# Kernel optimization log

Hardware: AMD Instinct MI355X
Metric: run time of the kernel (lower is better)

## Reference

```python
import jax, jax.numpy as jnp
import numpy as np
from jax import lax

S, B, T, H, FH, FU = 8, 256, 90, 256, 14, 76
IN_H, IN_F, IN_U = 16, 16, 4


def _cell(x, h, c, Wih, Whh, b):
    # x:[S,B,in] h,c:[S,B,H] Wih:[S,4H,in] Whh:[S,4H,H] b:[S,4H]
    g = jnp.einsum('sbi,sgi->sbg', x, Wih) + jnp.einsum('sbh,sgh->sbg', h, Whh) + b[:, None, :]
    i, f, gg, o = jnp.split(g, 4, axis=-1)
    c = jax.nn.sigmoid(f) * c + jax.nn.sigmoid(i) * jnp.tanh(gg)
    h = jax.nn.sigmoid(o) * jnp.tanh(c)
    return h, c


def _encode(x_seq, params):
    # x_seq:[T,S,B,in]; stacked LSTM, zero initial state (torch nn.LSTM default)
    hs, cs = [], []
    inp = x_seq
    for (Wih, Whh, b) in params:
        h0 = jnp.zeros((x_seq.shape[1], x_seq.shape[2], Whh.shape[-1]), x_seq.dtype)

        def step(carry, x, Wih=Wih, Whh=Whh, b=b):
            h, c = _cell(x, carry[0], carry[1], Wih, Whh, b)
            return (h, c), h

        (h, c), inp = lax.scan(step, (h0, h0), inp)
        hs.append(h); cs.append(c)
    return jnp.stack(hs), jnp.stack(cs)  # [L,S,B,H]


def _decode(x_seq, params, h0, c0, level, win, wout, gW, gb, adj, flow_std):
    L = len(params)

    def step(carry, x):
        hs, cs, lev = carry
        inp = x
        nh, nc = [], []
        for l in range(L):
            h, c = _cell(inp, hs[l], cs[l], *params[l])
            inp = h; nh.append(h); nc.append(c)
        # headers_in: Linear(H+1 -> H, no bias) + ReLU (dropout is eval no-op)
        feat = jnp.concatenate([inp, lev], axis=-1)            # [S,B,H+1]
        hin = jax.nn.relu(jnp.einsum('sbf,shf->sbh', feat, win))
        # GraphConvolution: adj @ (X W) + b over the site axis
        graphed = jnp.einsum('st,tbk->sbk', adj, jnp.einsum('sbh,hk->sbk', hin, gW)) + gb
        # headers_out: ReLU + Linear(H -> 1, no bias)
        flow = jnp.einsum('sbh,soh->sbo', jax.nn.relu(graphed), wout)  # [S,B,1]
        lev = lev + flow * flow_std[:, None, None]
        return (jnp.stack(nh), jnp.stack(nc), lev), flow[..., 0]
    (hs, cs, lev), flows = lax.scan(step, (h0, c0, level), x_seq)
    return hs, cs, lev, flows  # flows: [T,S,B]


def setup_inputs() -> dict:
    key = jax.random.key(0)
    ks = iter(jax.random.split(key, 40))
    sc = 1.0 / np.sqrt(H)

    def u(shape):
        return jax.random.uniform(next(ks), shape, jnp.float32, -sc, sc)

    inp = {
        'x_d': jax.random.normal(next(ks), (S, B, T, IN_H), jnp.float32),
        'x_f': jax.random.normal(next(ks), (S, B, FH, IN_F), jnp.float32),
        'x_ff': jax.random.normal(next(ks), (S, B, FU, IN_U), jnp.float32),
        'level0': jax.random.uniform(next(ks), (S, B, 1), jnp.float32),
        'flow_std': jax.random.uniform(next(ks), (S,), jnp.float32, 0.5, 2.0),
    }
    # adjacency: chain edges + self loops (diag=True, digraph=False)
    adj = np.zeros((S, S), dtype=np.float32)
    for i in range(S - 1):
        adj[i, i + 1] = 1.0
    adj += np.eye(S, dtype=np.float32)
    inp['adj'] = jnp.asarray(adj)
    for pfx, in0 in [('enc', IN_H), ('df', IN_F), ('du', IN_U)]:
        inp[pfx + '_Wih0'] = u((S, 4 * H, in0))
        inp[pfx + '_Whh0'] = u((S, 4 * H, H))
        inp[pfx + '_b0'] = u((S, 4 * H))
        inp[pfx + '_Wih1'] = u((S, 4 * H, H))
        inp[pfx + '_Whh1'] = u((S, 4 * H, H))
        inp[pfx + '_b1'] = u((S, 4 * H))
    inp['win'] = u((S, H, H + 1))
    inp['wout'] = u((S, 1, H))
    inp['gW'] = u((H, H))
    inp['gb'] = u((H,))
    return inp


def reference(x_d, x_f, x_ff, level0, flow_std, adj,
              enc_Wih0, enc_Whh0, enc_b0, enc_Wih1, enc_Whh1, enc_b1,
              df_Wih0, df_Whh0, df_b0, df_Wih1, df_Whh1, df_b1,
              du_Wih0, du_Whh0, du_b0, du_Wih1, du_Whh1, du_b1,
              win, wout, gW, gb):
    enc_p = [(enc_Wih0, enc_Whh0, enc_b0), (enc_Wih1, enc_Whh1, enc_b1)]
    df_p = [(df_Wih0, df_Whh0, df_b0), (df_Wih1, df_Whh1, df_b1)]
    du_p = [(du_Wih0, du_Whh0, du_b0), (du_Wih1, du_Whh1, du_b1)]
    # encode historic sequence per site
    h, c = _encode(jnp.transpose(x_d, (2, 0, 1, 3)), enc_p)
    # forecast-horizon decode with graph mixing each step
    h, c, lev, f1 = _decode(jnp.transpose(x_f, (2, 0, 1, 3)), df_p, h, c,
                            level0, win, wout, gW, gb, adj, flow_std)
    # future-horizon decode continues from the same state
    h, c, lev, f2 = _decode(jnp.transpose(x_ff, (2, 0, 1, 3)), du_p, h, c,
                            lev, win, wout, gW, gb, adj, flow_std)
    flows = jnp.concatenate([f1, f2], axis=0)      # [FH+FU, S, B]
    return jnp.transpose(flows, (2, 0, 1))         # [B, target_horizon, S]
```

## Files before the change

kernel.cpp:

```cpp
#include <hip/hip_runtime.h>

typedef unsigned short u16;
typedef __bf16 bf16_t;
typedef bf16_t bf16x8 __attribute__((ext_vector_type(8)));
typedef float f32x4 __attribute__((ext_vector_type(4)));
typedef unsigned int u32x4 __attribute__((ext_vector_type(4)));

#define DEV static __device__ __forceinline__

DEV u16 f2bf(float f){ unsigned u = __float_as_uint(f); return (u16)((u + 0x7fffu + ((u>>16)&1u))>>16); }
DEV float bf2f(u16 b){ return __uint_as_float(((unsigned)b)<<16); }
DEV float sigf(float x){ return 1.0f/(1.0f+__expf(-x)); }
DEV float tanhf_(float x){ float e = __expf(2.0f*x); return 1.0f - 2.0f/(e+1.0f); }

union FragU { bf16x8 v; u16 u[8]; u32x4 q; };

DEV void ldg16_nw(u32x4 r[16], const void* b0, const void* b1){
  asm volatile(
    "global_load_dwordx4 %0,  %16, off sc0 sc1\n\t"
    "global_load_dwordx4 %1,  %16, off offset:64 sc0 sc1\n\t"
    "global_load_dwordx4 %2,  %16, off offset:128 sc0 sc1\n\t"
    "global_load_dwordx4 %3,  %16, off offset:192 sc0 sc1\n\t"
    "global_load_dwordx4 %4,  %16, off offset:256 sc0 sc1\n\t"
    "global_load_dwordx4 %5,  %16, off offset:320 sc0 sc1\n\t"
    "global_load_dwordx4 %6,  %16, off offset:384 sc0 sc1\n\t"
    "global_load_dwordx4 %7,  %16, off offset:448 sc0 sc1\n\t"
    "global_load_dwordx4 %8,  %17, off sc0 sc1\n\t"
    "global_load_dwordx4 %9,  %17, off offset:64 sc0 sc1\n\t"
    "global_load_dwordx4 %10, %17, off offset:128 sc0 sc1\n\t"
    "global_load_dwordx4 %11, %17, off offset:192 sc0 sc1\n\t"
    "global_load_dwordx4 %12, %17, off offset:256 sc0 sc1\n\t"
    "global_load_dwordx4 %13, %17, off offset:320 sc0 sc1\n\t"
    "global_load_dwordx4 %14, %17, off offset:384 sc0 sc1\n\t"
    "global_load_dwordx4 %15, %17, off offset:448 sc0 sc1"
    : "=&v"(r[0]), "=&v"(r[1]), "=&v"(r[2]), "=&v"(r[3]),
      "=&v"(r[4]), "=&v"(r[5]), "=&v"(r[6]), "=&v"(r[7]),
      "=&v"(r[8]), "=&v"(r[9]), "=&v"(r[10]), "=&v"(r[11]),
      "=&v"(r[12]), "=&v"(r[13]), "=&v"(r[14]), "=&v"(r[15])
    : "v"(b0), "v"(b1)
    : "memory");
}
DEV void wait_vm16(){ asm volatile("s_waitcnt vmcnt(16)" ::: "memory"); __builtin_amdgcn_sched_barrier(0); }
DEV void wait_vm0(){ asm volatile("s_waitcnt vmcnt(0)" ::: "memory"); __builtin_amdgcn_sched_barrier(0); }

DEV void ldg8f_sc(u32x4 r[8], float& lv, const void* b0, const float* lp){
  asm volatile(
    "global_load_dwordx4 %0, %9, off sc0 sc1\n\t"
    "global_load_dwordx4 %1, %9, off offset:64 sc0 sc1\n\t"
    "global_load_dwordx4 %2, %9, off offset:128 sc0 sc1\n\t"
    "global_load_dwordx4 %3, %9, off offset:192 sc0 sc1\n\t"
    "global_load_dwordx4 %4, %9, off offset:256 sc0 sc1\n\t"
    "global_load_dwordx4 %5, %9, off offset:320 sc0 sc1\n\t"
    "global_load_dwordx4 %6, %9, off offset:384 sc0 sc1\n\t"
    "global_load_dwordx4 %7, %9, off offset:448 sc0 sc1\n\t"
    "global_load_dword %8, %10, off sc0 sc1\n\t"
    "s_waitcnt vmcnt(0)"
    : "=&v"(r[0]), "=&v"(r[1]), "=&v"(r[2]), "=&v"(r[3]),
      "=&v"(r[4]), "=&v"(r[5]), "=&v"(r[6]), "=&v"(r[7]), "=&v"(lv)
    : "v"(b0), "v"(lp)
    : "memory");
}
DEV float ldf_sc(const float* p){
  float r;
  asm volatile("global_load_dword %0, %1, off sc0 sc1\n\ts_waitcnt vmcnt(0)"
               : "=&v"(r) : "v"(p) : "memory");
  return r;
}
DEV void stg16_sc(void* p, u32x4 v){
  asm volatile("global_store_dwordx4 %0, %1, off sc0 sc1" :: "v"(p), "v"(v) : "memory");
}
DEV void stf_sc(float* p, float v){
  asm volatile("global_store_dword %0, %1, off sc0 sc1" :: "v"(p), "v"(v) : "memory");
}

struct PArgs {
  const u16 *whh0[3], *wih0p[3], *whh1[3], *wih1[3];
  const float *b0[3], *b1[3];
  const float *x[3];
  const u16 *winH; const float *winLev;
  const u16 *gT;
  const float *gb, *wout, *adj, *fstd;
  u16 *h0a, *h0b, *h1a, *h1b;
  u16 *hgA, *hgB;
  float *levA, *levB;
  float *out;
  unsigned *bar;
  int T[3]; int IN[3];
};

#define RLX __ATOMIC_RELAXED
#define AGT __HIP_MEMORY_SCOPE_AGENT

DEV void gsync_site(unsigned* cnt, unsigned gen){
  asm volatile("s_waitcnt vmcnt(0)" ::: "memory");
  __syncthreads();
  if (threadIdx.x == 0){
    __hip_atomic_fetch_add(cnt, 1u, RLX, AGT);
    unsigned tgt = gen * 32u;
    while (__hip_atomic_load(cnt, RLX, AGT) < tgt) __builtin_amdgcn_s_sleep(1);
  }
  __syncthreads();
}

DEV void gsync_glob(unsigned* bar, int s, bool leader, unsigned gen, unsigned ggen){
  asm volatile("s_waitcnt vmcnt(0)" ::: "memory");
  __syncthreads();
  if (threadIdx.x == 0){
    unsigned* cnt  = bar + s*64;
    unsigned* rel  = bar + 512 + s*64;
    unsigned* root = bar + 1024;
    __hip_atomic_fetch_add(cnt, 1u, RLX, AGT);
    if (leader){
      while (__hip_atomic_load(cnt, RLX, AGT) < gen*32u) __builtin_amdgcn_s_sleep(1);
      __hip_atomic_fetch_add(root, 1u, RLX, AGT);
      while (__hip_atomic_load(root, RLX, AGT) < ggen*8u) __builtin_amdgcn_s_sleep(1);
      __hip_atomic_store(rel, ggen, RLX, AGT);
    } else {
      while (__hip_atomic_load(rel, RLX, AGT) < ggen) __builtin_amdgcn_s_sleep(1);
    }
  }
  __syncthreads();
}

DEV void pinW256(const u16* Wsite, int gt, u16* lds, int tid){
#pragma unroll
  for (int it = 0; it < 8; ++it){
    int flat = it*512 + tid;
    int n = flat >> 5, ks = flat & 31;
    int j = (n >> 5)*256 + gt*32 + (n & 31);
    bf16x8 v = *reinterpret_cast<const bf16x8*>(Wsite + (size_t)j*256 + ks*8);
    int sl = ks ^ (n & 7);
    *reinterpret_cast<bf16x8*>(lds + n*256 + sl*8) = v;
  }
}
DEV void pinWp(const u16* wpSite, int gt, u16* lds, int tid){
  int n = tid >> 2, ks = tid & 3;
  int j = (n >> 5)*256 + gt*32 + (n & 31);
  bf16x8 v = *reinterpret_cast<const bf16x8*>(wpSite + (size_t)j*32 + ks*8);
  int sl = ks ^ (n & 3);
  *reinterpret_cast<bf16x8*>(lds + n*32 + sl*8) = v;
}
DEV void pinWin(const u16* winH, int s, int gt, u16* lds, int tid){
#pragma unroll
  for (int it = 0; it < 2; ++it){
    int flat = it*512 + tid;
    int nn = flat >> 5, ks = flat & 31;
    bf16x8 v = *reinterpret_cast<const bf16x8*>(winH + ((size_t)s*256 + gt*32 + nn)*256 + ks*8);
    int sl = ks ^ (nn & 7);
    *reinterpret_cast<bf16x8*>(lds + nn*256 + sl*8) = v;
  }
}

DEV void seg_mfma(const u16* ldsW, const u32x4 a[16], f32x4 acc[2][4],
                  int l15, int l4, int nh){
#pragma unroll
  for (int ck = 0; ck < 8; ++ck){
#pragma unroll
    for (int mf = 0; mf < 2; ++mf){
      FragU af; af.q = a[mf*8 + ck];
#pragma unroll
      for (int q = 0; q < 4; ++q){
        int n = q*32 + nh*16 + l15;
        int sl = (ck*4 + l4) ^ (n & 7);
        acc[mf][q] = __builtin_amdgcn_mfma_f32_16x16x32_bf16(
            af.v, *reinterpret_cast<const bf16x8*>(ldsW + n*256 + sl*8), acc[mf][q], 0,0,0);
      }
    }
  }
}

DEV void cell_epi2(const float bb[4], float* cR, u16* hOutSite,
                   int rowBase, int hcb, int lane, u16* wscr, const f32x4 acc[2][4]){
  int l15 = lane & 15, l4 = lane >> 4;
#pragma unroll
  for (int mf = 0; mf < 2; ++mf)
#pragma unroll
    for (int r = 0; r < 4; ++r){
      float gi = acc[mf][0][r] + bb[0];
      float gf = acc[mf][1][r] + bb[1];
      float gg = acc[mf][2][r] + bb[2];
      float go = acc[mf][3][r] + bb[3];
      float cn = sigf(gf)*cR[mf*4+r] + sigf(gi)*tanhf_(gg);
      cR[mf*4+r] = cn;
      wscr[(mf*16 + l4*4 + r)*16 + l15] = f2bf(sigf(go)*tanhf_(cn));
    }
  asm volatile("s_waitcnt lgkmcnt(0)" ::: "memory");
  u32x4 v = *reinterpret_cast<const u32x4*>(wscr + lane*8);
  stg16_sc(hOutSite + (size_t)(rowBase + (lane>>1))*256 + hcb + (lane&1)*8, v);
}

__global__ __launch_bounds__(512, 2) void k_persist(PArgs A){
  extern __shared__ char smem[];
  u16* lds0 = (u16*)smem;
  u16* lds1 = (u16*)(smem + 65536);
  u16* ldsWin = (u16*)(smem + 65536 + 8192);
  u16* scratch = (u16*)(smem + 131072);
  float (*red)[16] = (float(*)[16])(smem + 139264);

  const int bid = blockIdx.x, tid = threadIdx.x;
  const int w = tid >> 6, lane = tid & 63, l15 = lane & 15, l4 = lane >> 4;
  const int s = bid & 7, fam = (bid >> 3) & 1, sub = bid >> 4;
  const int bt = sub & 1, gt = sub >> 1;
  const int mt = w & 3, nh = w >> 2;
  const int rowBase = bt*128 + mt*32;
  const int hcb = gt*32 + nh*16;
  const size_t sOff = (size_t)s*65536;
  const bool leader = (bid < 8);
  unsigned* siteCnt = A.bar + s*64;
  u16* wscr = scratch + w*512;

  float cR[8];
#pragma unroll
  for (int i = 0; i < 8; ++i) cR[i] = 0.f;

  unsigned gen = 0, ggen = 0;
  const int gb0[3] = {0, 90, 104};

  for (int ph = 0; ph < 3; ++ph){
    const int T = A.T[ph];
    const int IN = A.IN[ph];
    const bool dec = (ph > 0);
    const int SS = T + (dec ? 3 : 1);
    const int tdb = (ph == 2) ? 14 : 0;

    float bb[4];
    if (fam == 0){
      pinW256(A.whh0[ph] + (size_t)s*262144, gt, lds0, tid);
      pinWp  (A.wih0p[ph] + (size_t)s*32768, gt, lds1, tid);
      pinWin (A.winH, s, gt, ldsWin, tid);
      const float* bS = A.b0[ph] + s*1024;
#pragma unroll
      for (int g = 0; g < 4; ++g) bb[g] = bS[g*256 + hcb + l15];
    } else {
      pinW256(A.whh1[ph] + (size_t)s*262144, gt, lds0, tid);
      pinW256(A.wih1[ph] + (size_t)s*262144, gt, lds1, tid);
      const float* bS = A.b1[ph] + s*1024;
#pragma unroll
      for (int g = 0; g < 4; ++g) bb[g] = bS[g*256 + hcb + l15];
    }
    __syncthreads();

    for (int ss = 0; ss < SS; ++ss){
      if (fam == 0){
        if (ss < T){
          int t = ss, g0 = gb0[ph] + t;
          const u16* h0in = ((g0 & 1) ? A.h0b : A.h0a) + sOff;
          u16* h0out = ((g0 & 1) ? A.h0a : A.h0b) + sOff;
          f32x4 acc[2][4];
#pragma unroll
          for (int mf = 0; mf < 2; ++mf)
#pragma unroll
            for (int q = 0; q < 4; ++q) acc[mf][q] = (f32x4){0.f,0.f,0.f,0.f};
          u32x4 a[16];
          ldg16_nw(a, h0in + (size_t)(rowBase + l15)*256 + l4*8,
                      h0in + (size_t)(rowBase + 16 + l15)*256 + l4*8);
          FragU xa[2];
#pragma unroll
          for (int mf = 0; mf < 2; ++mf){
#pragma unroll
            for (int e = 0; e < 8; ++e) xa[mf].u[e] = 0;
            const float* xrow = A.x[ph] + ((size_t)(s*256 + rowBase + mf*16 + l15)*T + t)*IN;
            if (IN == 16){
              if (l4 < 2){
                float4 u0 = reinterpret_cast<const float4*>(xrow)[l4*2];
                float4 u1 = reinterpret_cast<const float4*>(xrow)[l4*2+1];
                xa[mf].u[0]=f2bf(u0.x); xa[mf].u[1]=f2bf(u0.y); xa[mf].u[2]=f2bf(u0.z); xa[mf].u[3]=f2bf(u0.w);
                xa[mf].u[4]=f2bf(u1.x); xa[mf].u[5]=f2bf(u1.y); xa[mf].u[6]=f2bf(u1.z); xa[mf].u[7]=f2bf(u1.w);
              }
            } else {
              if (l4 == 0){
                float4 u0 = *reinterpret_cast<const float4*>(xrow);
                xa[mf].u[0]=f2bf(u0.x); xa[mf].u[1]=f2bf(u0.y); xa[mf].u[2]=f2bf(u0.z); xa[mf].u[3]=f2bf(u0.w);
              }
            }
          }
          wait_vm0();
          seg_mfma(lds0, a, acc, l15, l4, nh);
#pragma unroll
          for (int mf = 0; mf < 2; ++mf)
#pragma unroll
            for (int q = 0; q < 4; ++q){
              int n = q*32 + nh*16 + l15;
              int sl = l4 ^ (n & 3);
              acc[mf][q] = __builtin_amdgcn_mfma_f32_16x16x32_bf16(
                  xa[mf].v, *reinterpret_cast<const bf16x8*>(lds1 + n*32 + sl*8), acc[mf][q], 0,0,0);
            }
          cell_epi2(bb, cR, h0out, rowBase, hcb, lane, wscr, acc);
        }
        if (dec){
          int th = ss - 2;
          if (th >= 0 && th < T){
            int g = gb0[ph] + th, tdec = tdb + th;
            const u16* h1cur = ((g & 1) ? A.h1a : A.h1b) + sOff;
            u16* hg = ((tdec & 1) ? A.hgB : A.hgA) + sOff;
            f32x4 a2[2];
            a2[0] = (f32x4){0.f,0.f,0.f,0.f}; a2[1] = a2[0];
            u32x4 a[16];
            ldg16_nw(a, h1cur + (size_t)(rowBase + l15)*256 + l4*8,
                        h1cur + (size_t)(rowBase + 16 + l15)*256 + l4*8);
            wait_vm0();
#pragma unroll
            for (int ck = 0; ck < 8; ++ck)
#pragma unroll
              for (int mf = 0; mf < 2; ++mf){
                FragU af; af.q = a[mf*8 + ck];
                int n = nh*16 + l15;
                int sl = (ck*4 + l4) ^ (n & 7);
                a2[mf] = __builtin_amdgcn_mfma_f32_16x16x32_bf16(
                    af.v, *reinterpret_cast<const bf16x8*>(ldsWin + n*256 + sl*8), a2[mf], 0,0,0);
              }
#pragma unroll
            for (int mf = 0; mf < 2; ++mf)
#pragma unroll
              for (int r = 0; r < 4; ++r)
                wscr[(mf*16 + l4*4 + r)*16 + l15] = f2bf(a2[mf][r]);
            asm volatile("s_waitcnt lgkmcnt(0)" ::: "memory");
            u32x4 v = *reinterpret_cast<const u32x4*>(wscr + lane*8);
            stg16_sc(hg + (size_t)(rowBase + (lane>>1))*256 + hcb + (lane&1)*8, v);
          }
        }
      } else {
        int t = ss - 1;
        if (t >= 0 && t < T){
          int g = gb0[ph] + t;
          const u16* h1in = ((g & 1) ? A.h1b : A.h1a) + sOff;
          u16* h1out = ((g & 1) ? A.h1a : A.h1b) + sOff;
          const u16* h0cur = ((g & 1) ? A.h0a : A.h0b) + sOff;
          f32x4 acc[2][4];
#pragma unroll
          for (int mf = 0; mf < 2; ++mf)
#pragma unroll
            for (int q = 0; q < 4; ++q) acc[mf][q] = (f32x4){0.f,0.f,0.f,0.f};
          u32x4 a0[16], a1[16];
          ldg16_nw(a0, h1in + (size_t)(rowBase + l15)*256 + l4*8,
                       h1in + (size_t)(rowBase + 16 + l15)*256 + l4*8);
          ldg16_nw(a1, h0cur + (size_t)(rowBase + l15)*256 + l4*8,
                       h0cur + (size_t)(rowBase + 16 + l15)*256 + l4*8);
          wait_vm16();
          seg_mfma(lds0, a0, acc, l15, l4, nh);
          wait_vm0();
          seg_mfma(lds1, a1, acc, l15, l4, nh);
          cell_epi2(bb, cR, h1out, rowBase, hcb, lane, wscr, acc);
        }
        if (dec){
          int tgl = ss - 3;
          if (tgl >= 0 && tgl < T){
            int tg = tdb + tgl;
            const u16* hgb16 = (tg & 1) ? A.hgB : A.hgA;
            const float* levc = (tg & 1) ? A.levB : A.levA;
            float* levn = (tg & 1) ? A.levA : A.levB;
            int brow0 = sub*16;
            f32x4 acc[2];
            acc[0] = (f32x4){0.f,0.f,0.f,0.f}; acc[1] = acc[0];
            for (int ts = 0; ts < 8; ++ts){
              float av = A.adj[s*8 + ts];
              if (av == 0.f) continue;
              float lv;
              u32x4 hv[8];
              ldg8f_sc(hv, lv, hgb16 + (size_t)ts*65536 + (size_t)(brow0 + l15)*256 + l4*8,
                       levc + ts*256 + brow0 + l15);
              const float* wlB = A.winLev + ts*256 + l4*8;
#pragma unroll
              for (int ck = 0; ck < 8; ++ck){
                FragU hr; hr.q = hv[ck];
                float4 w0 = *reinterpret_cast<const float4*>(wlB + ck*32);
                float4 w1 = *reinterpret_cast<const float4*>(wlB + ck*32 + 4);
                float wls[8] = {w0.x,w0.y,w0.z,w0.w,w1.x,w1.y,w1.z,w1.w};
                FragU af;
#pragma unroll
                for (int e = 0; e < 8; ++e)
                  af.u[e] = f2bf(fmaxf(bf2f(hr.u[e]) + lv*wls[e], 0.f) * av);
#pragma unroll
                for (int q = 0; q < 2; ++q){
                  int n = (w*2+q)*16 + l15;
                  bf16x8 bfr = *reinterpret_cast<const bf16x8*>(A.gT + (size_t)n*256 + ck*32 + l4*8);
                  acc[q] = __builtin_amdgcn_mfma_f32_16x16x32_bf16(af.v, bfr, acc[q], 0,0,0);
                }
              }
            }
            float part[4] = {0.f,0.f,0.f,0.f};
            const float* woS = A.wout + s*256;
#pragma unroll
            for (int q = 0; q < 2; ++q){
              int m = (w*2+q)*16 + l15;
              float gbv = A.gb[m], wo = woS[m];
#pragma unroll
              for (int r = 0; r < 4; ++r) part[r] += fmaxf(acc[q][r] + gbv, 0.f) * wo;
            }
#pragma unroll
            for (int d = 1; d < 16; d <<= 1)
#pragma unroll
              for (int r = 0; r < 4; ++r) part[r] += __shfl_xor(part[r], d, 64);
            if (l15 == 0)
#pragma unroll
              for (int r = 0; r < 4; ++r) red[w][l4*4+r] = part[r];
            __syncthreads();
            if (tid < 16){
              float flow = 0.f;
#pragma unroll
              for (int ww = 0; ww < 8; ++ww) flow += red[ww][tid];
              int b = brow0 + tid;
              A.out[(size_t)b*720 + tg*8 + s] = flow;
              float lvo = ldf_sc(levc + s*256 + b);
              stf_sc(levn + s*256 + b, lvo + flow * A.fstd[s]);
            }
          }
        }
      }
      ++gen;
      if (dec){ ++ggen; gsync_glob(A.bar, s, leader, gen, ggen); }
      else     gsync_site(siteCnt, gen);
    }
  }
}

struct Cvt9Args { const float* s[9]; u16* d[9]; };
__global__ void k_cvt9(Cvt9Args A){
  size_t i = (size_t)blockIdx.x*256 + threadIdx.x;
  int t = (int)(i >> 21); size_t r = i & 2097151u;
  A.d[t][r] = f2bf(A.s[t][r]);
}
struct Pad3Args { const float* s[3]; u16* d[3]; int kx[3]; };
__global__ void k_pad3(Pad3Args A){
  size_t i = (size_t)blockIdx.x*256 + threadIdx.x;
  int t = (int)(i >> 18); int r = (int)(i & 262143u);
  int row = r >> 5, col = r & 31;
  int kx = A.kx[t];
  A.d[t][r] = (col < kx) ? f2bf(A.s[t][(size_t)row*kx + col]) : (u16)0;
}
__global__ void k_win(const float* win, u16* winH, float* winLev){
  size_t i = (size_t)blockIdx.x*256 + threadIdx.x;
  if (i >= (size_t)8*256*257) return;
  int k = (int)(i % 257); size_t sm = i / 257;
  float v = win[i];
  if (k < 256) winH[sm*256 + k] = f2bf(v);
  else winLev[sm] = v;
}
__global__ void k_gt(const float* gW, u16* gT){
  int i = blockIdx.x*256 + threadIdx.x;
  int h = i >> 8, k = i & 255;
  gT[(size_t)k*256 + h] = f2bf(gW[i]);
}

extern "C" void kernel_launch(void* const* d_in, const int* in_sizes, int n_in,
                              void* d_out, int out_size, void* d_ws, size_t ws_size,
                              hipStream_t stream){
  const float* x_d    = (const float*)d_in[0];
  const float* x_f    = (const float*)d_in[1];
  const float* x_ff   = (const float*)d_in[2];
  const float* level0 = (const float*)d_in[3];
  const float* fstd   = (const float*)d_in[4];
  const float* adj    = (const float*)d_in[5];
  const float* W[18];
  for (int i = 0; i < 18; i++) W[i] = (const float*)d_in[6+i];
  const float* win  = (const float*)d_in[24];
  const float* wout = (const float*)d_in[25];
  const float* gW   = (const float*)d_in[26];
  const float* gb   = (const float*)d_in[27];

  char* base = (char*)d_ws;
  size_t off = 0;
  auto alloc = [&](size_t bytes)->void*{
    void* r = base + off;
    off += (bytes + 255) & ~(size_t)255;
    return r;
  };
  u16* wb[9]; for (int i = 0; i < 9; i++) wb[i] = (u16*)alloc((size_t)2097152*2);
  u16* wp[3]; for (int i = 0; i < 3; i++) wp[i] = (u16*)alloc((size_t)262144*2);
  u16* winH = (u16*)alloc((size_t)524288*2);
  u16* gT   = (u16*)alloc((size_t)65536*2);
  float* winLev = (float*)alloc((size_t)2048*4);
  u16* h0a = (u16*)alloc((size_t)524288*2);
  u16* h0b = (u16*)alloc((size_t)524288*2);
  u16* h1a = (u16*)alloc((size_t)524288*2);
  u16* h1b = (u16*)alloc((size_t)524288*2);
  u16* hgA = (u16*)alloc((size_t)524288*2);
  u16* hgB = (u16*)alloc((size_t)524288*2);
  float* levA = (float*)alloc((size_t)2048*4);
  float* levB = (float*)alloc((size_t)2048*4);
  unsigned* bar = (unsigned*)alloc(8192);

  Cvt9Args c9;
  const float* c9s[9] = { W[1], W[4], W[3],  W[7], W[10], W[9],  W[13], W[16], W[15] };
  for (int i = 0; i < 9; i++){ c9.s[i] = c9s[i]; c9.d[i] = wb[i]; }
  k_cvt9<<<73728,256,0,stream>>>(c9);

  Pad3Args p3;
  const float* p3s[3] = { W[0], W[6], W[12] };
  int kx3[3] = {16,16,4};
  for (int i = 0; i < 3; i++){ p3.s[i] = p3s[i]; p3.d[i] = wp[i]; p3.kx[i] = kx3[i]; }
  k_pad3<<<3072,256,0,stream>>>(p3);

  k_win<<<2057,256,0,stream>>>(win, winH, winLev);
  k_gt<<<256,256,0,stream>>>(gW, gT);

  (void)hipMemsetAsync(h0a, 0, (size_t)524288*2, stream);
  (void)hipMemsetAsync(h1a, 0, (size_t)524288*2, stream);
  (void)hipMemsetAsync(bar, 0, 8192, stream);
  (void)hipMemcpyAsync(levA, level0, (size_t)2048*4, hipMemcpyDeviceToDevice, stream);

  PArgs A;
  for (int ph = 0; ph < 3; ++ph){
    A.whh0[ph] = wb[ph*3+0];
    A.whh1[ph] = wb[ph*3+1];
    A.wih1[ph] = wb[ph*3+2];
    A.wih0p[ph] = wp[ph];
  }
  A.b0[0] = W[2];  A.b1[0] = W[5];
  A.b0[1] = W[8];  A.b1[1] = W[11];
  A.b0[2] = W[14]; A.b1[2] = W[17];
  A.x[0] = x_d; A.x[1] = x_f; A.x[2] = x_ff;
  A.winH = winH; A.winLev = winLev;
  A.gT = gT; A.gb = gb; A.wout = wout; A.adj = adj; A.fstd = fstd;
  A.h0a = h0a; A.h0b = h0b; A.h1a = h1a; A.h1b = h1b;
  A.hgA = hgA; A.hgB = hgB;
  A.levA = levA; A.levB = levB;
  A.out = (float*)d_out;
  A.bar = bar;
  A.T[0] = 90; A.T[1] = 14; A.T[2] = 76;
  A.IN[0] = 16; A.IN[1] = 16; A.IN[2] = 4;

  const int smemBytes = 139776;
  (void)hipFuncSetAttribute((const void*)k_persist, hipFuncAttributeMaxDynamicSharedMemorySize, smemBytes);
  k_persist<<<dim3(256), dim3(512), smemBytes, stream>>>(A);
}
```

Measured before the change: 3.328 ms.

## Replace global/site barriers with fine-grained dependency counters per site and batch half

Replaces the per-step site barrier and the two-level global barrier with per-(site, batch-half, family) arrival counters. At the start of each step, one wavefront polls only the counters its work depends on: its own site, plus the neighbouring site during decode, following the graph and layer data flow. This is meant to cut the cost of an all-to-all barrier on each of the 90+ recurrent steps and let independent groups run ahead. It depends on the dependency sets being complete, and a missing edge would cause a race.

```diff
diff --git a/kernel.cpp b/kernel.cpp
--- a/kernel.cpp
+++ b/kernel.cpp
@@ -7,6 +7,8 @@
 typedef unsigned int u32x4 __attribute__((ext_vector_type(4)));
 
 #define DEV static __device__ __forceinline__
+#define RLX __ATOMIC_RELAXED
+#define AGT __HIP_MEMORY_SCOPE_AGENT
 
 DEV u16 f2bf(float f){ unsigned u = __float_as_uint(f); return (u16)((u + 0x7fffu + ((u>>16)&1u))>>16); }
 DEV float bf2f(u16 b){ return __uint_as_float(((unsigned)b)<<16); }
@@ -57,8 +59,7 @@
     "s_waitcnt vmcnt(0)"
     : "=&v"(r[0]), "=&v"(r[1]), "=&v"(r[2]), "=&v"(r[3]),
       "=&v"(r[4]), "=&v"(r[5]), "=&v"(r[6]), "=&v"(r[7]), "=&v"(lv)
-    : "v"(b0), "v"(lp)
-    : "memory");
+    : "v"(b0), "v"(lp) : "memory");
 }
 DEV float ldf_sc(const float* p){
   float r;
@@ -71,6 +72,12 @@
 }
 DEV void stf_sc(float* p, float v){
   asm volatile("global_store_dword %0, %1, off sc0 sc1" :: "v"(p), "v"(v) : "memory");
+}
+DEV unsigned ld_spin_ic(const unsigned* p){
+  unsigned r;
+  asm volatile("global_load_dword %0, %1, off sc0 sc1\n\ts_waitcnt vmcnt(0)"
+               : "=&v"(r) : "v"(p) : "memory");
+  return r;
 }
 
 struct PArgs {
@@ -88,40 +95,6 @@
   int T[3]; int IN[3];
 };
 
-#define RLX __ATOMIC_RELAXED
-#define AGT __HIP_MEMORY_SCOPE_AGENT
-
-DEV void gsync_site(unsigned* cnt, unsigned gen){
-  asm volatile("s_waitcnt vmcnt(0)" ::: "memory");
-  __syncthreads();
-  if (threadIdx.x == 0){
-    __hip_atomic_fetch_add(cnt, 1u, RLX, AGT);
-    unsigned tgt = gen * 32u;
-    while (__hip_atomic_load(cnt, RLX, AGT) < tgt) __builtin_amdgcn_s_sleep(1);
-  }
-  __syncthreads();
-}
-
-DEV void gsync_glob(unsigned* bar, int s, bool leader, unsigned gen, unsigned ggen){
-  asm volatile("s_waitcnt vmcnt(0)" ::: "memory");
-  __syncthreads();
-  if (threadIdx.x == 0){
-    unsigned* cnt  = bar + s*64;
-    unsigned* rel  = bar + 512 + s*64;
-    unsigned* root = bar + 1024;
-    __hip_atomic_fetch_add(cnt, 1u, RLX, AGT);
-    if (leader){
-      while (__hip_atomic_load(cnt, RLX, AGT) < gen*32u) __builtin_amdgcn_s_sleep(1);
-      __hip_atomic_fetch_add(root, 1u, RLX, AGT);
-      while (__hip_atomic_load(root, RLX, AGT) < ggen*8u) __builtin_amdgcn_s_sleep(1);
-      __hip_atomic_store(rel, ggen, RLX, AGT);
-    } else {
-      while (__hip_atomic_load(rel, RLX, AGT) < ggen) __builtin_amdgcn_s_sleep(1);
-    }
-  }
-  __syncthreads();
-}
-
 DEV void pinW256(const u16* Wsite, int gt, u16* lds, int tid){
 #pragma unroll
   for (int it = 0; it < 8; ++it){
@@ -196,6 +169,7 @@
   u16* ldsWin = (u16*)(smem + 65536 + 8192);
   u16* scratch = (u16*)(smem + 131072);
   float (*red)[16] = (float(*)[16])(smem + 139264);
+  __shared__ unsigned pollE[8], pollD[8];
 
   const int bid = blockIdx.x, tid = threadIdx.x;
   const int w = tid >> 6, lane = tid & 63, l15 = lane & 15, l4 = lane >> 4;
@@ -205,15 +179,40 @@
   const int rowBase = bt*128 + mt*32;
   const int hcb = gt*32 + nh*16;
   const size_t sOff = (size_t)s*65536;
-  const bool leader = (bid < 8);
-  unsigned* siteCnt = A.bar + s*64;
   u16* wscr = scratch + w*512;
 
+  auto offA = [](int ss, int bb){ return (unsigned)((ss*2 + bb)*64); };
+  auto offB = [](int ss, int bb){ return (unsigned)(1024 + (ss*2 + bb)*64); };
+  if (tid == 0){
+    pollE[0] = offA(s, bt); pollE[1] = offB(s, bt);
+#pragma unroll
+    for (int i = 2; i < 8; ++i) pollE[i] = pollE[0];
+    if (fam == 0){
+      pollD[0] = offA(s, bt);
+      pollD[1] = offB(s, 0); pollD[2] = offB(s, 1);
+      pollD[3] = (s > 0) ? offB(s-1, 0) : pollD[0];
+      pollD[4] = (s > 0) ? offB(s-1, 1) : pollD[0];
+      pollD[5] = pollD[0]; pollD[6] = pollD[0]; pollD[7] = pollD[0];
+    } else {
+      pollD[0] = offA(s, 0); pollD[1] = offA(s, 1);
+      pollD[2] = offB(s, 0); pollD[3] = offB(s, 1);
+      if (s < 7){
+        pollD[4] = offA(s+1, 0); pollD[5] = offA(s+1, 1);
+        pollD[6] = offB(s+1, 0); pollD[7] = offB(s+1, 1);
+      } else {
+        pollD[4] = pollD[0]; pollD[5] = pollD[0];
+        pollD[6] = pollD[0]; pollD[7] = pollD[0];
+      }
+    }
+  }
+  unsigned* myCnt = A.bar + ((fam == 0) ? offA(s, bt) : offB(s, bt));
+  __syncthreads();
+
   float cR[8];
 #pragma unroll
   for (int i = 0; i < 8; ++i) cR[i] = 0.f;
 
-  unsigned gen = 0, ggen = 0;
+  unsigned gen = 0;
   const int gb0[3] = {0, 90, 104};
 
   for (int ph = 0; ph < 3; ++ph){
@@ -241,6 +240,18 @@
     __syncthreads();
 
     for (int ss = 0; ss < SS; ++ss){
+      if (w == 0){
+        unsigned off = (dec ? pollD : pollE)[lane & 7];
+        const unsigned* p = A.bar + off;
+        unsigned tgt = 8u * gen;
+        for (;;){
+          unsigned v = ld_spin_ic(p);
+          if (__all((int)(v >= tgt))) break;
+          __builtin_amdgcn_s_sleep(1);
+        }
+      }
+      __syncthreads();
+
       if (fam == 0){
         if (ss < T){
           int t = ss, g0 = gb0[ph] + t;
@@ -407,9 +418,10 @@
           }
         }
       }
+      asm volatile("s_waitcnt vmcnt(0)" ::: "memory");
+      __syncthreads();
+      if (tid == 0) __hip_atomic_fetch_add(myCnt, 1u, RLX, AGT);
       ++gen;
-      if (dec){ ++ggen; gsync_glob(A.bar, s, leader, gen, ggen); }
-      else     gsync_site(siteCnt, gen);
     }
   }
 }
@@ -478,7 +490,7 @@
   u16* hgB = (u16*)alloc((size_t)524288*2);
   float* levA = (float*)alloc((size_t)2048*4);
   float* levB = (float*)alloc((size_t)2048*4);
-  unsigned* bar = (unsigned*)alloc(8192);
+  unsigned* bar = (unsigned*)alloc(16384);
 
   Cvt9Args c9;
   const float* c9s[9] = { W[1], W[4], W[3],  W[7], W[10], W[9],  W[13], W[16], W[15] };
@@ -496,7 +508,7 @@
 
   (void)hipMemsetAsync(h0a, 0, (size_t)524288*2, stream);
   (void)hipMemsetAsync(h1a, 0, (size_t)524288*2, stream);
-  (void)hipMemsetAsync(bar, 0, 8192, stream);
+  (void)hipMemsetAsync(bar, 0, 16384, stream);
   (void)hipMemcpyAsync(levA, level0, (size_t)2048*4, hipMemcpyDeviceToDevice, stream);
 
   PArgs A;
```

New measurement: 3.235 ms. 1.03x faster.
